# Kernel optimization log

Measured on AMD Instinct MI355X. Metric: run time of the kernel, lower is better.

## Reference

```python
import jax, jax.numpy as jnp
import numpy as np

DIM = 192
HEADS = 6
HEAD_DIM = DIM // HEADS
WS = 8
SHIFT = WS // 2
B, H, W = 32, 64, 64
EPS = 1e-5


def _rel_pos_index(ws):
    coords = np.stack(np.meshgrid(np.arange(ws), np.arange(ws), indexing='ij'))  # [2,ws,ws]
    cf = coords.reshape(2, -1)  # [2,N]
    rel = cf[:, :, None] - cf[:, None, :]  # [2,N,N]
    rel = rel.transpose(1, 2, 0)
    rel[:, :, 0] += ws - 1
    rel[:, :, 1] += ws - 1
    rel[:, :, 0] *= 2 * ws - 1
    return jnp.asarray(rel.sum(-1))  # [N,N] int32


def _shift_mask(Hp, Wp, ws, shift):
    img = np.zeros((Hp, Wp))
    slices = (slice(0, -ws), slice(-ws, -shift), slice(-shift, None))
    cnt = 0
    for hs in slices:
        for wsl in slices:
            img[hs, wsl] = cnt
            cnt += 1
    m = img.reshape(Hp // ws, ws, Wp // ws, ws).transpose(0, 2, 1, 3).reshape(-1, ws * ws)
    diff = m[:, None, :] - m[:, :, None]
    return jnp.asarray(np.where(diff != 0, -100.0, 0.0).astype(np.float32))  # [nW,N,N]


def _layernorm(x, g, b):
    mu = x.mean(-1, keepdims=True)
    var = ((x - mu) ** 2).mean(-1, keepdims=True)
    return (x - mu) / jnp.sqrt(var + EPS) * g + b


def _win_part(x, ws):
    b, h, w, c = x.shape
    x = x.reshape(b, h // ws, ws, w // ws, ws, c).transpose(0, 1, 3, 2, 4, 5)
    return x.reshape(-1, ws * ws, c)


def _win_rev(win, ws, h, w):
    b = win.shape[0] // (h * w // ws // ws)
    x = win.reshape(b, h // ws, w // ws, ws, ws, -1).transpose(0, 1, 3, 2, 4, 5)
    return x.reshape(b, h, w, -1)


def setup_inputs() -> dict:
    key = jax.random.key(0)
    ks = jax.random.split(key, 6)
    d = DIM
    init = lambda k, shape, scale: jax.random.normal(k, shape, jnp.float32) * scale
    return {
        'x': jax.random.normal(ks[0], (B, H, W, d), jnp.float32),
        'ln1_g': jnp.ones((d,), jnp.float32),
        'ln1_b': jnp.zeros((d,), jnp.float32),
        'qkv_w': init(ks[1], (3 * d, d), 0.02),
        'qkv_b': jnp.zeros((3 * d,), jnp.float32),
        'proj_w': init(ks[2], (d, d), 0.02),
        'proj_b': jnp.zeros((d,), jnp.float32),
        'rel_bias_table': init(ks[3], ((2 * WS - 1) ** 2, HEADS), 0.02),
        'ln2_g': jnp.ones((d,), jnp.float32),
        'ln2_b': jnp.zeros((d,), jnp.float32),
        'mlp_w1': init(ks[4], (4 * d, d), 0.02),
        'mlp_b1': jnp.zeros((4 * d,), jnp.float32),
        'mlp_w2': init(ks[5], (d, 4 * d), 0.02),
        'mlp_b2': jnp.zeros((d,), jnp.float32),
    }


def reference(x, ln1_g, ln1_b, qkv_w, qkv_b, proj_w, proj_b, rel_bias_table, ln2_g, ln2_b, mlp_w1, mlp_b1, mlp_w2, mlp_b2):
    b, h, w, c = x.shape
    N = WS * WS
    shortcut = x
    y = _layernorm(x, ln1_g, ln1_b)
    # shifted window: roll, partition
    y = jnp.roll(y, shift=(-SHIFT, -SHIFT), axis=(1, 2))
    xw = _win_part(y, WS)  # [B_, N, C]
    B_ = xw.shape[0]
    qkv = (xw @ qkv_w.T + qkv_b).reshape(B_, N, 3, HEADS, HEAD_DIM)
    q, k, v = qkv[:, :, 0], qkv[:, :, 1], qkv[:, :, 2]  # [B_, N, H, hd]
    scale = HEAD_DIM ** -0.5
    attn = jnp.einsum('bnhd,bmhd->bhnm', q * scale, k)  # [B_, H, N, N]
    rel = rel_bias_table[_rel_pos_index(WS)]  # [N, N, heads]
    attn = attn + rel.transpose(2, 0, 1)[None]
    mask = _shift_mask(h, w, WS, SHIFT)  # [nW, N, N]
    nW = mask.shape[0]
    attn = attn.reshape(B_ // nW, nW, HEADS, N, N) + mask[None, :, None]
    attn = jax.nn.softmax(attn.reshape(B_, HEADS, N, N), axis=-1)
    out = jnp.einsum('bhnm,bmhd->bnhd', attn, v).reshape(B_, N, c)
    out = out @ proj_w.T + proj_b
    y = _win_rev(out, WS, h, w)
    y = jnp.roll(y, shift=(SHIFT, SHIFT), axis=(1, 2))
    x2 = shortcut + y
    z = _layernorm(x2, ln2_g, ln2_b)
    z = jax.nn.gelu(z @ mlp_w1.T + mlp_b1, approximate=False) @ mlp_w2.T + mlp_b2
    return x2 + z
```

## Files before the change

### kernel.cpp

```cpp
#include <hip/hip_runtime.h>
#include <hip/hip_bf16.h>

typedef __bf16 bf16_t;
typedef __bf16 bf16x8 __attribute__((ext_vector_type(8)));
typedef float f32x4 __attribute__((ext_vector_type(4)));

#define MFMA16x16(a, b, c) __builtin_amdgcn_mfma_f32_16x16x32_bf16((a), (b), (c), 0, 0, 0)

constexpr int DIM = 192;
constexpr int NHEAD = 6;
constexpr int NWIN = 2048;
constexpr int WTOK = 64;


__global__ __launch_bounds__(256) void cvt_qkvwf(const float* __restrict__ s, bf16_t* __restrict__ d) {
    const int t = blockIdx.x * 256 + threadIdx.x;
    if (t >= 216 * 64) return;
    const int lane = t & 63, f = t >> 6;
    const int nt = f & 1, kk = (f >> 1) % 6, ph = f / 12;
    const int row = ph * 32 + nt * 16 + (lane & 15);
    const int col = kk * 32 + (lane >> 4) * 8;
    const float* sp = s + row * 192 + col;
    bf16_t* dp = d + (size_t)t * 8;
#pragma unroll
    for (int e = 0; e < 8; ++e) dp[e] = (bf16_t)sp[e];
}

__global__ __launch_bounds__(256) void cvt_projwf(const float* __restrict__ s, bf16_t* __restrict__ d) {
    const int t = blockIdx.x * 256 + threadIdx.x;
    if (t >= 72 * 64) return;
    const int lane = t & 63, f = t >> 6;
    const int nt = f % 3, kk = (f / 3) % 6, wv = f / 18;
    const int row = wv * 48 + nt * 16 + (lane & 15);
    const int col = kk * 32 + (lane >> 4) * 8;
    const float* sp = s + row * 192 + col;
    bf16_t* dp = d + (size_t)t * 8;
#pragma unroll
    for (int e = 0; e < 8; ++e) dp[e] = (bf16_t)sp[e];
}

__global__ __launch_bounds__(256) void cvt_w1f(const float* __restrict__ s, bf16_t* __restrict__ d) {
    const int t = blockIdx.x * 256 + threadIdx.x;
    if (t >= 288 * 64) return;
    const int lane = t & 63, f = t >> 6;
    const int nt = f % 3, kk = (f / 3) % 6, q = f / 18;
    const int wv = q & 3, kc = q >> 2;
    const int row = kc * 192 + wv * 48 + nt * 16 + (lane & 15);
    const int col = kk * 32 + (lane >> 4) * 8;
    const float* sp = s + row * 192 + col;
    bf16_t* dp = d + (size_t)t * 8;
#pragma unroll
    for (int e = 0; e < 8; ++e) dp[e] = (bf16_t)sp[e];
}

__global__ __launch_bounds__(256) void cvt_w2f(const float* __restrict__ s, bf16_t* __restrict__ d) {
    const int t = blockIdx.x * 256 + threadIdx.x;
    if (t >= 288 * 64) return;
    const int lane = t & 63, f = t >> 6;
    const int nt = f % 3, kk = (f / 3) % 6, q = f / 18;
    const int wv = q & 3, kc = q >> 2;
    const int row = wv * 48 + nt * 16 + (lane & 15);
    const int col = kc * 192 + kk * 32 + (lane >> 4) * 8;
    const float* sp = s + row * 768 + col;
    bf16_t* dp = d + (size_t)t * 8;
#pragma unroll
    for (int e = 0; e < 8; ++e) dp[e] = (bf16_t)sp[e];
}

__global__ __launch_bounds__(256) void ln_win_kernel(const float* __restrict__ in,
                                                     const float* __restrict__ g,
                                                     const float* __restrict__ bta,
                                                     bf16_t* __restrict__ ywf) {
    __shared__ bf16_t y_s[64][200];
    const int tid = threadIdx.x, lane = tid & 63, wv = tid >> 6;
    const int win = blockIdx.x;
    const int b_ = win >> 6, hb = (win >> 3) & 7, wb = win & 7;
    const float gv0 = g[lane], gv1 = g[lane + 64], gv2 = g[lane + 128];
    const float bv0 = bta[lane], bv1 = bta[lane + 64], bv2 = bta[lane + 128];
    for (int i = 0; i < 16; ++i) {
        const int n = wv * 16 + i;
        const int th = n >> 3, tw = n & 7;
        const int hh = (hb * 8 + th + 4) & 63;
        const int ww = (wb * 8 + tw + 4) & 63;
        const size_t src = ((size_t)(b_ * 64 + hh) * 64 + ww) * DIM;
        const float v0 = in[src + lane], v1 = in[src + lane + 64], v2 = in[src + lane + 128];
        float sm = v0 + v1 + v2;
        float q = v0 * v0 + v1 * v1 + v2 * v2;
#pragma unroll
        for (int m = 1; m < 64; m <<= 1) {
            sm += __shfl_xor(sm, m);
            q += __shfl_xor(q, m);
        }
        const float mu = sm * (1.0f / DIM);
        const float inv = rsqrtf(q * (1.0f / DIM) - mu * mu + 1e-5f);
        y_s[n][lane]       = (bf16_t)((v0 - mu) * inv * gv0 + bv0);
        y_s[n][lane + 64]  = (bf16_t)((v1 - mu) * inv * gv1 + bv1);
        y_s[n][lane + 128] = (bf16_t)((v2 - mu) * inv * gv2 + bv2);
    }
    __syncthreads();
    bf16_t* dst = ywf + (size_t)win * 12288;
    for (int j = tid; j < 1536; j += 256) {
        const int f = j >> 6, ln = j & 63;
        const int mt = f & 3, kk = f >> 2;
        const int row = mt * 16 + (ln & 15), col = kk * 32 + (ln >> 4) * 8;
        *reinterpret_cast<bf16x8*>(dst + (size_t)j * 8) =
            *reinterpret_cast<const bf16x8*>(&y_s[row][col]);
    }
}

__global__ __launch_bounds__(64, 3) void attn_kernel(const bf16_t* __restrict__ ywf,
                                                     const bf16_t* __restrict__ qkvwf,
                                                     const float* __restrict__ qkvb,
                                                     const float* __restrict__ relb,
                                                     bf16_t* __restrict__ aout) {
    __shared__ bf16_t scr[6400];
    const int lane = threadIdx.x;
    const int l15 = lane & 15, l4 = lane >> 4;
    const int wh = (blockIdx.x & 7) * ((NWIN * NHEAD) >> 3) + (blockIdx.x >> 3);
    const int win = wh / 6;
    const int h = wh - win * 6;
    const bf16_t* ywin = ywf + (size_t)win * 12288;

    bf16_t* tb = scr;
    bf16_t* vtb = scr + 4096;

    auto part_gemm = [&](int ph, f32x4 (&acc)[4][2]) {
#pragma unroll
        for (int kk = 0; kk < 6; ++kk) {
            bf16x8 a[4], b[2];
#pragma unroll
            for (int mt = 0; mt < 4; ++mt)
                a[mt] = *reinterpret_cast<const bf16x8*>(ywin + ((kk * 4 + mt) << 9) + lane * 8);
#pragma unroll
            for (int nt = 0; nt < 2; ++nt)
                b[nt] = *reinterpret_cast<const bf16x8*>(
                    qkvwf + (size_t)((((ph * 6 + kk) << 1) + nt) << 9) + lane * 8);
#pragma unroll
            for (int mt = 0; mt < 4; ++mt)
#pragma unroll
                for (int nt = 0; nt < 2; ++nt)
                    acc[mt][nt] = MFMA16x16(a[mt], b[nt], acc[mt][nt]);
        }
    };

    {
        f32x4 acc[4][2] = {};
        const int ph = 12 + h;
        part_gemm(ph, acc);
#pragma unroll
        for (int nt = 0; nt < 2; ++nt) {
            const int d = nt * 16 + l15;
            const float bias = qkvb[ph * 32 + d];
#pragma unroll
            for (int mt = 0; mt < 4; ++mt)
#pragma unroll
                for (int r = 0; r < 4; ++r)
                    vtb[d * 72 + mt * 16 + l4 * 4 + r] = (bf16_t)(acc[mt][nt][r] + bias);
        }
    }
    {
        f32x4 acc[4][2] = {};
        const int ph = h;
        part_gemm(ph, acc);
#pragma unroll
        for (int nt = 0; nt < 2; ++nt) {
            const int d = nt * 16 + l15;
            const float bias = qkvb[ph * 32 + d];
#pragma unroll
            for (int mt = 0; mt < 4; ++mt)
#pragma unroll
                for (int r = 0; r < 4; ++r)
                    tb[(mt * 16 + l4 * 4 + r) * 40 + d] =
                        (bf16_t)((acc[mt][nt][r] + bias) * 0.17677669529663689f);
        }
    }
    bf16x8 aq[4];
#pragma unroll
    for (int mt = 0; mt < 4; ++mt)
        aq[mt] = *reinterpret_cast<const bf16x8*>(&tb[(mt * 16 + l15) * 40 + l4 * 8]);

    {
        f32x4 acc[4][2] = {};
        const int ph = 6 + h;
        part_gemm(ph, acc);
#pragma unroll
        for (int nt = 0; nt < 2; ++nt) {
            const int d = nt * 16 + l15;
            const float bias = qkvb[ph * 32 + d];
#pragma unroll
            for (int mt = 0; mt < 4; ++mt)
#pragma unroll
                for (int r = 0; r < 4; ++r)
                    tb[(mt * 16 + l4 * 4 + r) * 40 + d] = (bf16_t)(acc[mt][nt][r] + bias);
        }
    }
    bf16x8 bk[4];
#pragma unroll
    for (int nt = 0; nt < 4; ++nt)
        bk[nt] = *reinterpret_cast<const bf16x8*>(&tb[(nt * 16 + l15) * 40 + l4 * 8]);

    f32x4 s[4][4] = {};
#pragma unroll
    for (int mt = 0; mt < 4; ++mt)
#pragma unroll
        for (int nt = 0; nt < 4; ++nt)
            s[mt][nt] = MFMA16x16(aq[mt], bk[nt], s[mt][nt]);

    const int hb = (win >> 3) & 7, wb = win & 7;
    int colc[4], colreg[4];
#pragma unroll
    for (int nt = 0; nt < 4; ++nt) {
        const int m = nt * 16 + l15;
        const int mh = m >> 3, mw = m & 7;
        colc[nt] = mh * 15 + mw;
        const int gh = hb * 8 + mh, gw = wb * 8 + mw;
        const int rh = (gh < 56) ? 0 : ((gh < 60) ? 1 : 2);
        const int rw = (gw < 56) ? 0 : ((gw < 60) ? 1 : 2);
        colreg[nt] = rh * 3 + rw;
    }
#pragma unroll
    for (int mt = 0; mt < 4; ++mt) {
#pragma unroll
        for (int r = 0; r < 4; ++r) {
            const int n = mt * 16 + l4 * 4 + r;
            const int nh = n >> 3, nw = n & 7;
            const int rowc = nh * 15 + nw + 112;
            const int gh = hb * 8 + nh, gw = wb * 8 + nw;
            const int rh = (gh < 56) ? 0 : ((gh < 60) ? 1 : 2);
            const int rw = (gw < 56) ? 0 : ((gw < 60) ? 1 : 2);
            const int rreg = rh * 3 + rw;
            float vals[4];
            float mx = -1e30f;
#pragma unroll
            for (int nt = 0; nt < 4; ++nt) {
                float v = s[mt][nt][r] + relb[(rowc - colc[nt]) * NHEAD + h];
                if (rreg != colreg[nt]) v -= 100.0f;
                vals[nt] = v;
                mx = fmaxf(mx, v);
            }
            mx = fmaxf(mx, __shfl_xor(mx, 1));
            mx = fmaxf(mx, __shfl_xor(mx, 2));
            mx = fmaxf(mx, __shfl_xor(mx, 4));
            mx = fmaxf(mx, __shfl_xor(mx, 8));
            float sum = 0.f;
#pragma unroll
            for (int nt = 0; nt < 4; ++nt) {
                vals[nt] = __expf(vals[nt] - mx);
                sum += vals[nt];
            }
            sum += __shfl_xor(sum, 1);
            sum += __shfl_xor(sum, 2);
            sum += __shfl_xor(sum, 4);
            sum += __shfl_xor(sum, 8);
            const float inv = 1.0f / sum;
            const int nsw = n & 7;
#pragma unroll
            for (int nt = 0; nt < 4; ++nt) {
                const int tk = nt * 16 + l15;
                tb[n * 64 + (((tk >> 3) ^ nsw) << 3) + (tk & 7)] = (bf16_t)(vals[nt] * inv);
            }
        }
    }

    f32x4 o[4][2] = {};
#pragma unroll
    for (int kk = 0; kk < 2; ++kk) {
        bf16x8 a[4], b[2];
#pragma unroll
        for (int mt = 0; mt < 4; ++mt) {
            const int tq = mt * 16 + l15;
            a[mt] = *reinterpret_cast<const bf16x8*>(&tb[tq * 64 + (((kk * 4 + l4) ^ (tq & 7)) << 3)]);
        }
#pragma unroll
        for (int nt = 0; nt < 2; ++nt)
            b[nt] = *reinterpret_cast<const bf16x8*>(&vtb[(nt * 16 + l15) * 72 + kk * 32 + l4 * 8]);
#pragma unroll
        for (int mt = 0; mt < 4; ++mt)
#pragma unroll
            for (int nt = 0; nt < 2; ++nt)
                o[mt][nt] = MFMA16x16(a[mt], b[nt], o[mt][nt]);
    }
    bf16_t* op = aout + (size_t)win * (WTOK * DIM) + h * 32;
#pragma unroll
    for (int mt = 0; mt < 4; ++mt)
#pragma unroll
        for (int nt = 0; nt < 2; ++nt)
#pragma unroll
            for (int r = 0; r < 4; ++r) {
                const int n = mt * 16 + l4 * 4 + r;
                op[n * DIM + nt * 16 + l15] = (bf16_t)o[mt][nt][r];
            }
}

__global__ __launch_bounds__(256) void proj_kernel(const bf16_t* __restrict__ ain,
                                                   const bf16_t* __restrict__ pwf,
                                                   const float* __restrict__ pbias,
                                                   const float* __restrict__ x,
                                                   float* __restrict__ x2) {
    __shared__ bf16_t a_s[64][200];
    const int tid = threadIdx.x;
    const int lane = tid & 63;
    const int wv = tid >> 6;
    const int win = blockIdx.x;
    const int l15 = lane & 15, l4 = lane >> 4;

    const bf16_t* asrc = ain + (size_t)win * (WTOK * DIM);
    for (int i = tid; i < WTOK * DIM / 8; i += 256) {
        const int idx = i * 8;
        *reinterpret_cast<bf16x8*>(&a_s[idx / DIM][idx % DIM]) =
            *reinterpret_cast<const bf16x8*>(asrc + idx);
    }
    __syncthreads();

    const int n0 = wv * 48;
    f32x4 acc[4][3] = {};
    for (int kk = 0; kk < 6; ++kk) {
        const int c0 = kk * 32 + l4 * 8;
        bf16x8 a[4], b[3];
#pragma unroll
        for (int mt = 0; mt < 4; ++mt)
            a[mt] = *reinterpret_cast<const bf16x8*>(&a_s[mt * 16 + l15][c0]);
#pragma unroll
        for (int nt = 0; nt < 3; ++nt)
            b[nt] = *reinterpret_cast<const bf16x8*>(
                pwf + (size_t)(((wv * 6 + kk) * 3 + nt) << 9) + lane * 8);
#pragma unroll
        for (int mt = 0; mt < 4; ++mt)
#pragma unroll
            for (int nt = 0; nt < 3; ++nt)
                acc[mt][nt] = MFMA16x16(a[mt], b[nt], acc[mt][nt]);
    }
    const int b_ = win >> 6, hb = (win >> 3) & 7, wb = win & 7;
#pragma unroll
    for (int mt = 0; mt < 4; ++mt)
#pragma unroll
        for (int r = 0; r < 4; ++r) {
            const int n = mt * 16 + l4 * 4 + r;
            const int th = n >> 3, tw = n & 7;
            const int hh = (hb * 8 + th + 4) & 63;
            const int ww = (wb * 8 + tw + 4) & 63;
            const size_t row = ((size_t)(b_ * 64 + hh) * 64 + ww) * DIM;
#pragma unroll
            for (int nt = 0; nt < 3; ++nt) {
                const int col = n0 + nt * 16 + l15;
                x2[row + col] = acc[mt][nt][r] + pbias[col] + x[row + col];
            }
        }
}

__device__ __forceinline__ float gelu_f(float v) {
    const float x2 = v * v;
    const float inner = fmaf(0.044715f * x2, v, v);
    const float e = __expf(inner * 1.5957691216057308f);
    const float r = __builtin_amdgcn_rcpf(e + 1.0f);
    return v - v * r;
}

__global__ __launch_bounds__(256, 3) void mlp_kernel(const float* __restrict__ g,
                                                     const float* __restrict__ bta,
                                                     const bf16_t* __restrict__ w1f,
                                                     const float* __restrict__ b1,
                                                     const bf16_t* __restrict__ w2f,
                                                     const float* __restrict__ b2,
                                                     float* __restrict__ xout) {
    __shared__ bf16_t z_s[64][200];
    __shared__ bf16_t h_s[64][200];
    const int tid = threadIdx.x, lane = tid & 63, wv = tid >> 6;
    const int l15 = lane & 15, l4 = lane >> 4;
    const size_t t0 = (size_t)blockIdx.x * 64;
    const int n0 = wv * 48;

    {
        const float gv0 = g[lane], gv1 = g[lane + 64], gv2 = g[lane + 128];
        const float bv0 = bta[lane], bv1 = bta[lane + 64], bv2 = bta[lane + 128];
        for (int i = 0; i < 16; ++i) {
            const int n = wv * 16 + i;
            const size_t src = (t0 + n) * DIM;
            const float v0 = xout[src + lane], v1 = xout[src + lane + 64], v2 = xout[src + lane + 128];
            float sm = v0 + v1 + v2;
            float q = v0 * v0 + v1 * v1 + v2 * v2;
#pragma unroll
            for (int m = 1; m < 64; m <<= 1) {
                sm += __shfl_xor(sm, m);
                q += __shfl_xor(q, m);
            }
            const float mu = sm * (1.0f / DIM);
            const float inv = rsqrtf(q * (1.0f / DIM) - mu * mu + 1e-5f);
            z_s[n][lane]       = (bf16_t)((v0 - mu) * inv * gv0 + bv0);
            z_s[n][lane + 64]  = (bf16_t)((v1 - mu) * inv * gv1 + bv1);
            z_s[n][lane + 128] = (bf16_t)((v2 - mu) * inv * gv2 + bv2);
        }
    }
    __syncthreads();

    f32x4 acc_o[4][3] = {};
    for (int kc = 0; kc < 4; ++kc) {
        const int fb = (kc * 4 + wv) * 18;
        f32x4 hacc[4][3] = {};
#pragma unroll
        for (int kk = 0; kk < 6; ++kk) {
            const int c0 = kk * 32 + l4 * 8;
            bf16x8 a[4], b[3];
#pragma unroll
            for (int mt = 0; mt < 4; ++mt)
                a[mt] = *reinterpret_cast<const bf16x8*>(&z_s[mt * 16 + l15][c0]);
#pragma unroll
            for (int nt = 0; nt < 3; ++nt)
                b[nt] = *reinterpret_cast<const bf16x8*>(
                    w1f + (size_t)((fb + kk * 3 + nt) << 9) + lane * 8);
#pragma unroll
            for (int mt = 0; mt < 4; ++mt)
#pragma unroll
                for (int nt = 0; nt < 3; ++nt)
                    hacc[mt][nt] = MFMA16x16(a[mt], b[nt], hacc[mt][nt]);
        }
        __syncthreads();
#pragma unroll
        for (int mt = 0; mt < 4; ++mt)
#pragma unroll
            for (int r = 0; r < 4; ++r) {
                const int n = mt * 16 + l4 * 4 + r;
#pragma unroll
                for (int nt = 0; nt < 3; ++nt) {
                    const int col = n0 + nt * 16 + l15;
                    h_s[n][col] = (bf16_t)gelu_f(hacc[mt][nt][r] + b1[kc * 192 + col]);
                }
            }
        __syncthreads();
#pragma unroll
        for (int kk = 0; kk < 6; ++kk) {
            const int c0 = kk * 32 + l4 * 8;
            bf16x8 a[4], b[3];
#pragma unroll
            for (int mt = 0; mt < 4; ++mt)
                a[mt] = *reinterpret_cast<const bf16x8*>(&h_s[mt * 16 + l15][c0]);
#pragma unroll
            for (int nt = 0; nt < 3; ++nt)
                b[nt] = *reinterpret_cast<const bf16x8*>(
                    w2f + (size_t)((fb + kk * 3 + nt) << 9) + lane * 8);
#pragma unroll
            for (int mt = 0; mt < 4; ++mt)
#pragma unroll
                for (int nt = 0; nt < 3; ++nt)
                    acc_o[mt][nt] = MFMA16x16(a[mt], b[nt], acc_o[mt][nt]);
        }
    }
#pragma unroll
    for (int mt = 0; mt < 4; ++mt)
#pragma unroll
        for (int r = 0; r < 4; ++r) {
            const int n = mt * 16 + l4 * 4 + r;
            const size_t addr = (t0 + n) * DIM;
#pragma unroll
            for (int nt = 0; nt < 3; ++nt) {
                const int col = n0 + nt * 16 + l15;
                xout[addr + col] = acc_o[mt][nt][r] + b2[col] + xout[addr + col];
            }
        }
}

extern "C" void kernel_launch(void* const* d_in, const int* in_sizes, int n_in,
                              void* d_out, int out_size, void* d_ws, size_t ws_size,
                              hipStream_t stream) {
    const float* x      = (const float*)d_in[0];
    const float* ln1_g  = (const float*)d_in[1];
    const float* ln1_b  = (const float*)d_in[2];
    const float* qkv_w  = (const float*)d_in[3];
    const float* qkv_b  = (const float*)d_in[4];
    const float* proj_w = (const float*)d_in[5];
    const float* proj_b = (const float*)d_in[6];
    const float* relb   = (const float*)d_in[7];
    const float* ln2_g  = (const float*)d_in[8];
    const float* ln2_b  = (const float*)d_in[9];
    const float* mlp_w1 = (const float*)d_in[10];
    const float* mlp_b1 = (const float*)d_in[11];
    const float* mlp_w2 = (const float*)d_in[12];
    const float* mlp_b2 = (const float*)d_in[13];
    float* out = (float*)d_out;

    char* ws = (char*)d_ws;
    bf16_t* qkvwf = (bf16_t*)(ws + 0);
    bf16_t* pwf   = (bf16_t*)(ws + 221184);
    bf16_t* w1f   = (bf16_t*)(ws + 294912);
    bf16_t* w2f   = (bf16_t*)(ws + 589824);
    bf16_t* bufA  = (bf16_t*)(ws + 884736);
    bf16_t* bufB  = (bf16_t*)(ws + 884736 + 50331648);

    cvt_qkvwf<<<54, 256, 0, stream>>>(qkv_w, qkvwf);
    cvt_projwf<<<18, 256, 0, stream>>>(proj_w, pwf);
    cvt_w1f<<<72, 256, 0, stream>>>(mlp_w1, w1f);
    cvt_w2f<<<72, 256, 0, stream>>>(mlp_w2, w2f);

    ln_win_kernel<<<NWIN, 256, 0, stream>>>(x, ln1_g, ln1_b, bufA);
    attn_kernel<<<NWIN * NHEAD, 64, 0, stream>>>(bufA, qkvwf, qkv_b, relb, bufB);
    proj_kernel<<<NWIN, 256, 0, stream>>>(bufB, pwf, proj_b, x, out);
    mlp_kernel<<<2048, 256, 0, stream>>>(ln2_g, ln2_b, w1f, mlp_b1, w2f, mlp_b2, out);
}
```

Baseline: 340.9 us.

## Fuse window attention with output projection and transpose MLP first GEMM

Attention and the output projection now run in one kernel. Each block handles one window with six waves, one per head. Per-head outputs are staged in LDS and then projected, with each wave producing 32 output columns, which removes the bf16 intermediate buffer round trip through global memory and one kernel launch. The MLP first GEMM is transposed so weights act as the A operand, which lets GELU outputs be written to LDS as 4-wide vectors. The trade-off is a larger block, about 77KB of LDS per block, and extra barriers, which may lower occupancy compared with the old 64-thread attention blocks.

```diff
diff --git a/kernel.cpp b/kernel.cpp
--- a/kernel.cpp
+++ b/kernel.cpp
@@ -2,6 +2,7 @@
 #include <hip/hip_bf16.h>
 
 typedef __bf16 bf16_t;
+typedef __bf16 bf16x4 __attribute__((ext_vector_type(4)));
 typedef __bf16 bf16x8 __attribute__((ext_vector_type(8)));
 typedef float f32x4 __attribute__((ext_vector_type(4)));
 
@@ -30,8 +31,8 @@
     const int t = blockIdx.x * 256 + threadIdx.x;
     if (t >= 72 * 64) return;
     const int lane = t & 63, f = t >> 6;
-    const int nt = f % 3, kk = (f / 3) % 6, wv = f / 18;
-    const int row = wv * 48 + nt * 16 + (lane & 15);
+    const int nt = f & 1, kk = (f >> 1) % 6, h = f / 12;
+    const int row = h * 32 + nt * 16 + (lane & 15);
     const int col = kk * 32 + (lane >> 4) * 8;
     const float* sp = s + row * 192 + col;
     bf16_t* dp = d + (size_t)t * 8;
@@ -108,21 +109,24 @@
     }
 }
 
-__global__ __launch_bounds__(64, 3) void attn_kernel(const bf16_t* __restrict__ ywf,
-                                                     const bf16_t* __restrict__ qkvwf,
-                                                     const float* __restrict__ qkvb,
-                                                     const float* __restrict__ relb,
-                                                     bf16_t* __restrict__ aout) {
-    __shared__ bf16_t scr[6400];
-    const int lane = threadIdx.x;
+__global__ __launch_bounds__(384, 3) void attnproj_kernel(const bf16_t* __restrict__ ywf,
+                                                          const bf16_t* __restrict__ qkvwf,
+                                                          const float* __restrict__ qkvb,
+                                                          const float* __restrict__ relb,
+                                                          const bf16_t* __restrict__ pwf,
+                                                          const float* __restrict__ pbias,
+                                                          const float* __restrict__ x,
+                                                          float* __restrict__ x2) {
+    __shared__ bf16_t scr[NHEAD][6400];
+    const int tid = threadIdx.x;
+    const int lane = tid & 63;
+    const int h = tid >> 6;
     const int l15 = lane & 15, l4 = lane >> 4;
-    const int wh = (blockIdx.x & 7) * ((NWIN * NHEAD) >> 3) + (blockIdx.x >> 3);
-    const int win = wh / 6;
-    const int h = wh - win * 6;
+    const int win = (blockIdx.x & 7) * (NWIN >> 3) + (blockIdx.x >> 3);
     const bf16_t* ywin = ywf + (size_t)win * 12288;
 
-    bf16_t* tb = scr;
-    bf16_t* vtb = scr + 4096;
+    bf16_t* tb = &scr[h][0];
+    bf16_t* vtb = &scr[h][4096];
 
     auto part_gemm = [&](int ph, f32x4 (&acc)[4][2]) {
 #pragma unroll
@@ -280,7 +284,9 @@
             for (int nt = 0; nt < 2; ++nt)
                 o[mt][nt] = MFMA16x16(a[mt], b[nt], o[mt][nt]);
     }
-    bf16_t* op = aout + (size_t)win * (WTOK * DIM) + h * 32;
+
+    __syncthreads();
+    bf16_t* O_s = &scr[0][0];
 #pragma unroll
     for (int mt = 0; mt < 4; ++mt)
 #pragma unroll
@@ -288,49 +294,29 @@
 #pragma unroll
             for (int r = 0; r < 4; ++r) {
                 const int n = mt * 16 + l4 * 4 + r;
-                op[n * DIM + nt * 16 + l15] = (bf16_t)o[mt][nt][r];
-            }
-}
-
-__global__ __launch_bounds__(256) void proj_kernel(const bf16_t* __restrict__ ain,
-                                                   const bf16_t* __restrict__ pwf,
-                                                   const float* __restrict__ pbias,
-                                                   const float* __restrict__ x,
-                                                   float* __restrict__ x2) {
-    __shared__ bf16_t a_s[64][200];
-    const int tid = threadIdx.x;
-    const int lane = tid & 63;
-    const int wv = tid >> 6;
-    const int win = blockIdx.x;
-    const int l15 = lane & 15, l4 = lane >> 4;
-
-    const bf16_t* asrc = ain + (size_t)win * (WTOK * DIM);
-    for (int i = tid; i < WTOK * DIM / 8; i += 256) {
-        const int idx = i * 8;
-        *reinterpret_cast<bf16x8*>(&a_s[idx / DIM][idx % DIM]) =
-            *reinterpret_cast<const bf16x8*>(asrc + idx);
-    }
+                O_s[n * 200 + h * 32 + nt * 16 + l15] = (bf16_t)o[mt][nt][r];
+            }
     __syncthreads();
 
-    const int n0 = wv * 48;
-    f32x4 acc[4][3] = {};
+    f32x4 pacc[4][2] = {};
+#pragma unroll
     for (int kk = 0; kk < 6; ++kk) {
         const int c0 = kk * 32 + l4 * 8;
-        bf16x8 a[4], b[3];
+        bf16x8 a[4], b[2];
 #pragma unroll
         for (int mt = 0; mt < 4; ++mt)
-            a[mt] = *reinterpret_cast<const bf16x8*>(&a_s[mt * 16 + l15][c0]);
-#pragma unroll
-        for (int nt = 0; nt < 3; ++nt)
+            a[mt] = *reinterpret_cast<const bf16x8*>(&O_s[(mt * 16 + l15) * 200 + c0]);
+#pragma unroll
+        for (int nt = 0; nt < 2; ++nt)
             b[nt] = *reinterpret_cast<const bf16x8*>(
-                pwf + (size_t)(((wv * 6 + kk) * 3 + nt) << 9) + lane * 8);
+                pwf + (size_t)((((h * 6 + kk) << 1) + nt) << 9) + lane * 8);
 #pragma unroll
         for (int mt = 0; mt < 4; ++mt)
 #pragma unroll
-            for (int nt = 0; nt < 3; ++nt)
-                acc[mt][nt] = MFMA16x16(a[mt], b[nt], acc[mt][nt]);
-    }
-    const int b_ = win >> 6, hb = (win >> 3) & 7, wb = win & 7;
+            for (int nt = 0; nt < 2; ++nt)
+                pacc[mt][nt] = MFMA16x16(a[mt], b[nt], pacc[mt][nt]);
+    }
+    const int b_ = win >> 6;
 #pragma unroll
     for (int mt = 0; mt < 4; ++mt)
 #pragma unroll
@@ -341,9 +327,9 @@
             const int ww = (wb * 8 + tw + 4) & 63;
             const size_t row = ((size_t)(b_ * 64 + hh) * 64 + ww) * DIM;
 #pragma unroll
-            for (int nt = 0; nt < 3; ++nt) {
-                const int col = n0 + nt * 16 + l15;
-                x2[row + col] = acc[mt][nt][r] + pbias[col] + x[row + col];
+            for (int nt = 0; nt < 2; ++nt) {
+                const int col = h * 32 + nt * 16 + l15;
+                x2[row + col] = pacc[mt][nt][r] + pbias[col] + x[row + col];
             }
         }
 }
@@ -396,36 +382,41 @@
     f32x4 acc_o[4][3] = {};
     for (int kc = 0; kc < 4; ++kc) {
         const int fb = (kc * 4 + wv) * 18;
-        f32x4 hacc[4][3] = {};
+        f32x4 hacc[3][4] = {};
 #pragma unroll
         for (int kk = 0; kk < 6; ++kk) {
             const int c0 = kk * 32 + l4 * 8;
-            bf16x8 a[4], b[3];
-#pragma unroll
-            for (int mt = 0; mt < 4; ++mt)
-                a[mt] = *reinterpret_cast<const bf16x8*>(&z_s[mt * 16 + l15][c0]);
-#pragma unroll
-            for (int nt = 0; nt < 3; ++nt)
-                b[nt] = *reinterpret_cast<const bf16x8*>(
-                    w1f + (size_t)((fb + kk * 3 + nt) << 9) + lane * 8);
-#pragma unroll
-            for (int mt = 0; mt < 4; ++mt)
-#pragma unroll
-                for (int nt = 0; nt < 3; ++nt)
-                    hacc[mt][nt] = MFMA16x16(a[mt], b[nt], hacc[mt][nt]);
+            bf16x8 wa[3], zb[4];
+#pragma unroll
+            for (int m = 0; m < 3; ++m)
+                wa[m] = *reinterpret_cast<const bf16x8*>(
+                    w1f + (size_t)((fb + kk * 3 + m) << 9) + lane * 8);
+#pragma unroll
+            for (int n = 0; n < 4; ++n)
+                zb[n] = *reinterpret_cast<const bf16x8*>(&z_s[n * 16 + l15][c0]);
+#pragma unroll
+            for (int m = 0; m < 3; ++m)
+#pragma unroll
+                for (int n = 0; n < 4; ++n)
+                    hacc[m][n] = MFMA16x16(wa[m], zb[n], hacc[m][n]);
         }
         __syncthreads();
 #pragma unroll
-        for (int mt = 0; mt < 4; ++mt)
-#pragma unroll
-            for (int r = 0; r < 4; ++r) {
-                const int n = mt * 16 + l4 * 4 + r;
-#pragma unroll
-                for (int nt = 0; nt < 3; ++nt) {
-                    const int col = n0 + nt * 16 + l15;
-                    h_s[n][col] = (bf16_t)gelu_f(hacc[mt][nt][r] + b1[kc * 192 + col]);
-                }
-            }
+        for (int m = 0; m < 3; ++m) {
+            const int hcol0 = n0 + m * 16 + l4 * 4;
+            const float* bp = &b1[kc * 192 + hcol0];
+            const float b0 = bp[0], bb1 = bp[1], b2v = bp[2], b3 = bp[3];
+#pragma unroll
+            for (int n = 0; n < 4; ++n) {
+                const int token = n * 16 + l15;
+                bf16x4 qd;
+                qd[0] = (bf16_t)gelu_f(hacc[m][n][0] + b0);
+                qd[1] = (bf16_t)gelu_f(hacc[m][n][1] + bb1);
+                qd[2] = (bf16_t)gelu_f(hacc[m][n][2] + b2v);
+                qd[3] = (bf16_t)gelu_f(hacc[m][n][3] + b3);
+                *reinterpret_cast<bf16x4*>(&h_s[token][hcol0]) = qd;
+            }
+        }
         __syncthreads();
 #pragma unroll
         for (int kk = 0; kk < 6; ++kk) {
@@ -484,7 +475,6 @@
     bf16_t* w1f   = (bf16_t*)(ws + 294912);
     bf16_t* w2f   = (bf16_t*)(ws + 589824);
     bf16_t* bufA  = (bf16_t*)(ws + 884736);
-    bf16_t* bufB  = (bf16_t*)(ws + 884736 + 50331648);
 
     cvt_qkvwf<<<54, 256, 0, stream>>>(qkv_w, qkvwf);
     cvt_projwf<<<18, 256, 0, stream>>>(proj_w, pwf);
@@ -492,7 +482,6 @@
     cvt_w2f<<<72, 256, 0, stream>>>(mlp_w2, w2f);
 
     ln_win_kernel<<<NWIN, 256, 0, stream>>>(x, ln1_g, ln1_b, bufA);
-    attn_kernel<<<NWIN * NHEAD, 64, 0, stream>>>(bufA, qkvwf, qkv_b, relb, bufB);
-    proj_kernel<<<NWIN, 256, 0, stream>>>(bufB, pwf, proj_b, x, out);
+    attnproj_kernel<<<NWIN, 384, 0, stream>>>(bufA, qkvwf, qkv_b, relb, pwf, proj_b, x, out);
     mlp_kernel<<<2048, 256, 0, stream>>>(ln2_g, ln2_b, w1f, mlp_b1, w2f, mlp_b2, out);
 }
```

New measurement: 394.5 us. 15.7% more time.
